# Kernel tuning notes

Measured on AMD Instinct MI355X. Metric: run time of the kernel, lower is better.

Reference implementation:

```python
import jax, jax.numpy as jnp
import numpy as np

NA, NT = 50000, 100000          # address / transaction node counts
FA, FT = 128, 64                # raw feature dims per node type
HID, OUT, HEADS, NCLS = 128, 64, 8, 2
E1, E2 = 500000, 250000         # cross-type / same-type edge counts
NEG_SLOPE = 0.2
LN_EPS = 1e-5


def _edge_att(xs, xd, src, dst, a_s, a_d, n_dst):
    # xs: [Ns,H,D] projected src feats, xd: [Nd,H,D] projected dst feats
    alpha_s = (xs * a_s).sum(-1)                     # [Ns,H]
    alpha_d = (xd * a_d).sum(-1)                     # [Nd,H]
    alpha = alpha_s[src] + alpha_d[dst]              # [E,H]
    alpha = jnp.where(alpha > 0, alpha, NEG_SLOPE * alpha)  # leaky_relu(0.2)
    # segment softmax over incoming edges of each dst node
    m = jax.lax.stop_gradient(jax.ops.segment_max(alpha, dst, num_segments=n_dst))
    m = jnp.where(jnp.isfinite(m), m, 0.0)
    ex = jnp.exp(alpha - m[dst])
    denom = jax.ops.segment_sum(ex, dst, num_segments=n_dst)
    w = ex / jnp.maximum(denom[dst], 1e-16)          # [E,H]
    msg = xs[src] * w[:, :, None]                    # [E,H,D]
    out = jax.ops.segment_sum(msg, dst, num_segments=n_dst)
    return jax.nn.relu(out.reshape(n_dst, -1))       # [Nd, H*D] (HANConv relu per edge type)


def _group(outs, q, kW, kb):
    # semantic-level attention over metapaths; outs: [K,N,F]
    score = (jnp.tanh(outs @ kW + kb).mean(axis=1) * q).sum(-1)  # [K]
    attn = jax.nn.softmax(score)
    return jnp.einsum('k,knf->nf', attn, outs)


def _layer_norm(x, g, b):
    mu = x.mean(-1, keepdims=True)
    var = ((x - mu) ** 2).mean(-1, keepdims=True)
    return (x - mu) / jnp.sqrt(var + LN_EPS) * g + b


def _han_conv(xa, xt, edges, Wa, ba, Wt, bt, atts, q, kW, kb):
    C = Wa.shape[1]
    D = C // HEADS
    za = (xa @ Wa + ba).reshape(-1, HEADS, D)
    zt = (xt @ Wt + bt).reshape(-1, HEADS, D)
    (eat_s, eat_d), (eta_s, eta_d), (eaa_s, eaa_d), (ett_s, ett_d) = edges
    (as_at, ad_at), (as_ta, ad_ta), (as_aa, ad_aa), (as_tt, ad_tt) = atts
    o_at = _edge_att(za, zt, eat_s, eat_d, as_at, ad_at, zt.shape[0])  # -> transaction
    o_ta = _edge_att(zt, za, eta_s, eta_d, as_ta, ad_ta, za.shape[0])  # -> address
    o_aa = _edge_att(za, za, eaa_s, eaa_d, as_aa, ad_aa, za.shape[0])  # -> address
    o_tt = _edge_att(zt, zt, ett_s, ett_d, as_tt, ad_tt, zt.shape[0])  # -> transaction
    new_a = _group(jnp.stack([o_ta, o_aa]), q, kW, kb)
    new_t = _group(jnp.stack([o_at, o_tt]), q, kW, kb)
    return new_a, new_t


def _forward(x_address, x_transaction,
             W_a1, b_a1, W_t1, b_t1,
             as_at1, ad_at1, as_ta1, ad_ta1, as_aa1, ad_aa1, as_tt1, ad_tt1,
             k1_W, k1_b, q1,
             W_a2, b_a2, W_t2, b_t2,
             as_at2, ad_at2, as_ta2, ad_ta2, as_aa2, ad_aa2, as_tt2, ad_tt2,
             k2_W, k2_b, q2,
             ln1_g, ln1_b, ln2_g, ln2_b, lin_W, lin_b, edges):
    atts1 = ((as_at1, ad_at1), (as_ta1, ad_ta1), (as_aa1, ad_aa1), (as_tt1, ad_tt1))
    atts2 = ((as_at2, ad_at2), (as_ta2, ad_ta2), (as_aa2, ad_aa2), (as_tt2, ad_tt2))
    xa, xt = _han_conv(x_address, x_transaction, edges, W_a1, b_a1, W_t1, b_t1, atts1, q1, k1_W, k1_b)
    xa = jax.nn.relu(_layer_norm(xa, ln1_g, ln1_b))
    xt = jax.nn.relu(_layer_norm(xt, ln1_g, ln1_b))
    # dropout is identity in eval mode
    xa, xt = _han_conv(xa, xt, edges, W_a2, b_a2, W_t2, b_t2, atts2, q2, k2_W, k2_b)
    xa = jax.nn.relu(_layer_norm(xa, ln2_g, ln2_b))
    return xa @ lin_W + lin_b                          # [NA, NCLS]


def setup_inputs() -> dict:
    key = jax.random.key(0)
    ks = jax.random.split(key, 40)
    D1, D2 = HID // HEADS, OUT // HEADS
    def n(i, shape, s=0.1):
        return jax.random.normal(ks[i], shape, jnp.float32) * s
    inp = {
        'x_address': jax.random.normal(ks[0], (NA, FA), jnp.float32),
        'x_transaction': jax.random.normal(ks[1], (NT, FT), jnp.float32),
        'eat_src': jax.random.randint(ks[2], (E1,), 0, NA),
        'eat_dst': jax.random.randint(ks[3], (E1,), 0, NT),
        'eta_src': jax.random.randint(ks[4], (E1,), 0, NT),
        'eta_dst': jax.random.randint(ks[5], (E1,), 0, NA),
        'eaa_src': jax.random.randint(ks[6], (E2,), 0, NA),
        'eaa_dst': jax.random.randint(ks[7], (E2,), 0, NA),
        'ett_src': jax.random.randint(ks[8], (E2,), 0, NT),
        'ett_dst': jax.random.randint(ks[9], (E2,), 0, NT),
        'W_a1': n(10, (FA, HID)), 'b_a1': jnp.zeros((HID,), jnp.float32),
        'W_t1': n(11, (FT, HID)), 'b_t1': jnp.zeros((HID,), jnp.float32),
        'as_at1': n(12, (HEADS, D1)), 'ad_at1': n(13, (HEADS, D1)),
        'as_ta1': n(14, (HEADS, D1)), 'ad_ta1': n(15, (HEADS, D1)),
        'as_aa1': n(16, (HEADS, D1)), 'ad_aa1': n(17, (HEADS, D1)),
        'as_tt1': n(18, (HEADS, D1)), 'ad_tt1': n(19, (HEADS, D1)),
        'k1_W': n(20, (HID, HID)), 'k1_b': jnp.zeros((HID,), jnp.float32), 'q1': n(21, (HID,)),
        'W_a2': n(22, (HID, OUT)), 'b_a2': jnp.zeros((OUT,), jnp.float32),
        'W_t2': n(23, (HID, OUT)), 'b_t2': jnp.zeros((OUT,), jnp.float32),
        'as_at2': n(24, (HEADS, D2)), 'ad_at2': n(25, (HEADS, D2)),
        'as_ta2': n(26, (HEADS, D2)), 'ad_ta2': n(27, (HEADS, D2)),
        'as_aa2': n(28, (HEADS, D2)), 'ad_aa2': n(29, (HEADS, D2)),
        'as_tt2': n(30, (HEADS, D2)), 'ad_tt2': n(31, (HEADS, D2)),
        'k2_W': n(32, (OUT, OUT)), 'k2_b': jnp.zeros((OUT,), jnp.float32), 'q2': n(33, (OUT,)),
        'ln1_g': jnp.ones((HID,), jnp.float32), 'ln1_b': jnp.zeros((HID,), jnp.float32),
        'ln2_g': jnp.ones((OUT,), jnp.float32), 'ln2_b': jnp.zeros((OUT,), jnp.float32),
        'lin_W': n(34, (OUT, NCLS)), 'lin_b': jnp.zeros((NCLS,), jnp.float32),
    }
    return inp


def reference(x_address, x_transaction,
              eat_src, eat_dst, eta_src, eta_dst, eaa_src, eaa_dst, ett_src, ett_dst,
              W_a1, b_a1, W_t1, b_t1,
              as_at1, ad_at1, as_ta1, ad_ta1, as_aa1, ad_aa1, as_tt1, ad_tt1,
              k1_W, k1_b, q1,
              W_a2, b_a2, W_t2, b_t2,
              as_at2, ad_at2, as_ta2, ad_ta2, as_aa2, ad_aa2, as_tt2, ad_tt2,
              k2_W, k2_b, q2,
              ln1_g, ln1_b, ln2_g, ln2_b, lin_W, lin_b):
    edges = ((eat_src, eat_dst), (eta_src, eta_dst), (eaa_src, eaa_dst), (ett_src, ett_dst))
    return _forward(x_address, x_transaction,
                    W_a1, b_a1, W_t1, b_t1,
                    as_at1, ad_at1, as_ta1, ad_ta1, as_aa1, ad_aa1, as_tt1, ad_tt1,
                    k1_W, k1_b, q1,
                    W_a2, b_a2, W_t2, b_t2,
                    as_at2, ad_at2, as_ta2, ad_ta2, as_aa2, ad_aa2, as_tt2, ad_tt2,
                    k2_W, k2_b, q2,
                    ln1_g, ln1_b, ln2_g, ln2_b, lin_W, lin_b, edges)
```

## Files before the change

kernel.cpp:

```cpp
#include <hip/hip_runtime.h>
#include <cstdint>
#include <cstddef>
#include <type_traits>

#define NA 50000
#define NT 100000
#define FA 128
#define FT 64
#define HID 128
#define OUTF 64
#define HEADS 8
#define E1 500000
#define E2 250000
#define NTOT (2*NT + 2*NA)
#define ETOT (2*E1 + 2*E2)
#define NSH 8

typedef __attribute__((ext_vector_type(8))) short short8;
typedef __attribute__((ext_vector_type(4))) float f32x4;

static __device__ __forceinline__ ushort f2b(float f) {
  unsigned int u = __float_as_uint(f);
  return (ushort)((u + 0x7fffu + ((u >> 16) & 1u)) >> 16);
}
static __device__ __forceinline__ float b2f(ushort b) {
  return __uint_as_float(((unsigned int)b) << 16);
}
static __device__ __forceinline__ float u2f_lo(unsigned int u) {
  return __uint_as_float(u << 16);
}
static __device__ __forceinline__ float u2f_hi(unsigned int u) {
  return __uint_as_float(u & 0xffff0000u);
}

template<int KK>
static __device__ __forceinline__ int lidx(int row, int off) {
  return row * KK + (off ^ ((row & 7) << 3));
}

template<int KK, int M>
static __device__ __forceinline__ void stageB(const float* __restrict__ W,
                                              ushort* __restrict__ Bls)
{
  constexpr int TPC = 256 / M;
  constexpr int CH  = KK / TPC;
  constexpr int BL  = (CH < 16) ? CH : 16;
  int t = threadIdx.x;
  int col = t % M;
  int k0 = (t / M) * CH;
  const float* Wp = W + col;
#pragma unroll
  for (int b = 0; b < CH; b += BL) {
    float v[BL];
#pragma unroll
    for (int i = 0; i < BL; i++) v[i] = Wp[(size_t)(k0 + b + i) * M];
#pragma unroll
    for (int q = 0; q < BL / 8; q++) {
      union { ushort u[8]; uint4 x; } p;
#pragma unroll
      for (int i = 0; i < 8; i++) p.u[i] = f2b(v[q * 8 + i]);
      *reinterpret_cast<uint4*>(&Bls[lidx<KK>(col, k0 + b + q * 8)]) = p.x;
    }
  }
}

template<int KK, typename AT>
struct ARegs {
  float4 f[std::is_same<AT, float>::value ? KK / 16 : 1];
  uint4  u[std::is_same<AT, float>::value ? 1 : KK / 32];
};

template<int KK, typename AT>
static __device__ __forceinline__ void loadA(const AT* __restrict__ A, int N,
                                             int row0, ARegs<KK, AT>& R)
{
  int t = threadIdx.x;
  int arow = t >> 2, ac0 = (t & 3) * (KK / 4);
  int row = row0 + arow;
  bool ok = row < N;
  const AT* Ap = A + (size_t)row * KK + ac0;
  if constexpr (std::is_same<AT, float>::value) {
#pragma unroll
    for (int j = 0; j < KK / 16; j++)
      R.f[j] = ok ? *reinterpret_cast<const float4*>(Ap + j * 4)
                  : make_float4(0.f, 0.f, 0.f, 0.f);
  } else {
#pragma unroll
    for (int j = 0; j < KK / 32; j++)
      R.u[j] = ok ? *reinterpret_cast<const uint4*>(Ap + j * 8)
                  : make_uint4(0, 0, 0, 0);
  }
}

template<int KK, typename AT>
static __device__ __forceinline__ void writeA(const ARegs<KK, AT>& R,
                                              ushort* __restrict__ Als)
{
  int t = threadIdx.x;
  int arow = t >> 2, ac0 = (t & 3) * (KK / 4);
#pragma unroll
  for (int j = 0; j < KK / 32; j++) {
    uint4 w;
    if constexpr (std::is_same<AT, float>::value) {
      union { ushort u[8]; uint4 x; } p;
      float4 a0 = R.f[2 * j], a1 = R.f[2 * j + 1];
      p.u[0] = f2b(a0.x); p.u[1] = f2b(a0.y); p.u[2] = f2b(a0.z); p.u[3] = f2b(a0.w);
      p.u[4] = f2b(a1.x); p.u[5] = f2b(a1.y); p.u[6] = f2b(a1.z); p.u[7] = f2b(a1.w);
      w = p.x;
    } else {
      w = R.u[j];
    }
    *reinterpret_cast<uint4*>(&Als[lidx<KK>(arow, ac0 + j * 8)]) = w;
  }
}

template<int KK, int NCT>
static __device__ __forceinline__ void mfma_tile(const ushort* __restrict__ Als,
    const ushort* __restrict__ Bls, f32x4* acc)
{
  int lane = threadIdx.x & 63, w = threadIdx.x >> 6;
  int l15 = lane & 15, l4 = lane >> 4;
#pragma unroll
  for (int ks = 0; ks < KK / 32; ks++) {
    short8 af = *reinterpret_cast<const short8*>(
        &Als[lidx<KK>(16 * w + l15, ks * 32 + l4 * 8)]);
#pragma unroll
    for (int n = 0; n < NCT; n++) {
      short8 bf = *reinterpret_cast<const short8*>(
          &Bls[lidx<KK>(16 * n + l15, ks * 32 + l4 * 8)]);
      acc[n] = __builtin_amdgcn_mfma_f32_16x16x32_bf16(af, bf, acc[n], 0, 0, 0);
    }
  }
}

template<int NV, int DD, int KK, int M, int TPB, typename AT>
__global__ __launch_bounds__(256) void zgemm_k(
    const AT* __restrict__ A, const float* __restrict__ W,
    const float* __restrict__ bias,
    const float* __restrict__ v0, const float* __restrict__ v1,
    const float* __restrict__ v2, const float* __restrict__ v3,
    float* __restrict__ o0, float* __restrict__ o1,
    float* __restrict__ o2, float* __restrict__ o3,
    ushort* __restrict__ Cb, int N)
{
  constexpr int NCT = M / 16;
  __shared__ __align__(16) ushort Bls[M * KK];
  __shared__ __align__(16) ushort Als[64 * KK];
  int t = threadIdx.x, w = t >> 6, lane = t & 63;
  int l15 = lane & 15, l4 = lane >> 4;
  int ntiles = (N + 63) >> 6;
  int tile0 = blockIdx.x * TPB;
  int nt = min(TPB, ntiles - tile0);

  stageB<KK, M>(W, Bls);
  ARegs<KK, AT> R;
  loadA<KK, AT>(A, N, tile0 * 64, R);

  float bv[NCT], aw0[NCT], aw1[NCT], aw2[NCT], aw3[NCT];
#pragma unroll
  for (int n = 0; n < NCT; n++) {
    int col = 16 * n + l15;
    bv[n] = bias[col];
    int head = (DD == 16) ? n : (n * 2 + (l15 >> 3));
    int vi = head * DD + (l15 & (DD - 1));
    aw0[n] = v0[vi];
    aw1[n] = (NV > 1) ? v1[vi] : 0.f;
    aw2[n] = (NV > 2) ? v2[vi] : 0.f;
    aw3[n] = (NV > 3) ? v3[vi] : 0.f;
  }

  for (int i = 0; i < nt; i++) {
    int row0 = (tile0 + i) * 64;
    __syncthreads();
    writeA<KK, AT>(R, Als);
    __syncthreads();
    if (i + 1 < nt) loadA<KK, AT>(A, N, row0 + 64, R);
    f32x4 acc[NCT];
#pragma unroll
    for (int n = 0; n < NCT; n++) acc[n] = (f32x4){0.f, 0.f, 0.f, 0.f};
    mfma_tile<KK, NCT>(Als, Bls, acc);

#pragma unroll
    for (int n = 0; n < NCT; n++) {
      int col = 16 * n + l15;
      int head = (DD == 16) ? n : (n * 2 + (l15 >> 3));
#pragma unroll
      for (int r = 0; r < 4; r++) {
        int row = row0 + 16 * w + l4 * 4 + r;
        float v = acc[n][r] + bv[n];
        if (row < N) Cb[(size_t)row * M + col] = f2b(v);
        float a0 = v * aw0[n], a1 = v * aw1[n], a2 = v * aw2[n], a3 = v * aw3[n];
#pragma unroll
        for (int o = 1; o < DD; o <<= 1) {
          a0 += __shfl_xor(a0, o);
          if (NV > 1) a1 += __shfl_xor(a1, o);
          if (NV > 2) a2 += __shfl_xor(a2, o);
          if (NV > 3) a3 += __shfl_xor(a3, o);
        }
        if ((l15 & (DD - 1)) == 0 && row < N) {
          o0[(size_t)row * 8 + head] = a0;
          if (NV > 1) o1[(size_t)row * 8 + head] = a1;
          if (NV > 2) o2[(size_t)row * 8 + head] = a2;
          if (NV > 3) o3[(size_t)row * 8 + head] = a3;
        }
      }
    }
  }
}

template<int KK, int M, int TPB>
__global__ __launch_bounds__(256) void score_k(
    const ushort* __restrict__ A0, const ushort* __restrict__ A1,
    const ushort* __restrict__ A2, const ushort* __restrict__ A3,
    const float* __restrict__ W, const float* __restrict__ bias,
    const float* __restrict__ qv, float* __restrict__ scp,
    int4 cumB, int4 Ns)
{
  constexpr int NCT = M / 16;
  __shared__ __align__(16) ushort Bls[M * KK];
  __shared__ __align__(16) ushort Als[64 * KK];
  __shared__ float red[4];
  int b = blockIdx.x;
  int tsk, bbase, N; const ushort* A;
  if      (b < cumB.x) { tsk = 0; bbase = 0;      N = Ns.x; A = A0; }
  else if (b < cumB.y) { tsk = 1; bbase = cumB.x; N = Ns.y; A = A1; }
  else if (b < cumB.z) { tsk = 2; bbase = cumB.y; N = Ns.z; A = A2; }
  else                 { tsk = 3; bbase = cumB.z; N = Ns.w; A = A3; }
  int t = threadIdx.x, w = t >> 6, lane = t & 63;
  int l15 = lane & 15, l4 = lane >> 4;
  int ntiles = (N + 63) >> 6;
  int tile0 = (b - bbase) * TPB;
  int nt = min(TPB, ntiles - tile0);

  stageB<KK, M>(W, Bls);
  ARegs<KK, ushort> R;
  loadA<KK, ushort>(A, N, tile0 * 64, R);

  float bb[NCT], qb[NCT];
#pragma unroll
  for (int n = 0; n < NCT; n++) {
    int col = 16 * n + l15;
    bb[n] = bias[col]; qb[n] = qv[col];
  }

  float ls = 0.f;
  for (int i = 0; i < nt; i++) {
    int row0 = (tile0 + i) * 64;
    __syncthreads();
    writeA<KK, ushort>(R, Als);
    __syncthreads();
    if (i + 1 < nt) loadA<KK, ushort>(A, N, row0 + 64, R);
    f32x4 acc[NCT];
#pragma unroll
    for (int n = 0; n < NCT; n++) acc[n] = (f32x4){0.f, 0.f, 0.f, 0.f};
    mfma_tile<KK, NCT>(Als, Bls, acc);
#pragma unroll
    for (int n = 0; n < NCT; n++) {
#pragma unroll
      for (int r = 0; r < 4; r++) {
        int row = row0 + 16 * w + l4 * 4 + r;
        if (row < N) ls += tanhf(acc[n][r] + bb[n]) * qb[n];
      }
    }
  }
#pragma unroll
  for (int o = 32; o > 0; o >>= 1) ls += __shfl_xor(ls, o);
  if (lane == 0) red[w] = ls;
  __syncthreads();
  if (t == 0) atomicAdd(&scp[tsk], red[0] + red[1] + red[2] + red[3]);
}

__global__ void hist4_sh(const int* __restrict__ d0, const int* __restrict__ d1,
    const int* __restrict__ d2, const int* __restrict__ d3,
    int* __restrict__ cnt8, float* __restrict__ scp)
{
  if (blockIdx.x == 0 && threadIdx.x < 8) scp[threadIdx.x] = 0.f;
  int e = blockIdx.x * 256 + threadIdx.x;
  int sh = blockIdx.x & (NSH - 1);
  int d;
  if      (e < E1)          d = d0[e];
  else if (e < 2*E1)        d = d1[e - E1] + NT;
  else if (e < 2*E1 + E2)   d = d2[e - 2*E1] + NT + NA;
  else if (e < ETOT)        d = d3[e - 2*E1 - E2] + NT + 2*NA;
  else return;
  atomicAdd(&cnt8[sh * NTOT + d], 1);
}

__global__ void scatter_sh(const int* __restrict__ s0, const int* __restrict__ d0,
    const int* __restrict__ s1, const int* __restrict__ d1,
    const int* __restrict__ s2, const int* __restrict__ d2,
    const int* __restrict__ s3, const int* __restrict__ d3,
    int* __restrict__ cur8, int* __restrict__ ssh)
{
  int e = blockIdx.x * 256 + threadIdx.x;
  int sh = blockIdx.x & (NSH - 1);
  int d, s;
  if      (e < E1)          { d = d0[e];                           s = s0[e]; }
  else if (e < 2*E1)        { d = d1[e - E1] + NT;                 s = s1[e - E1]; }
  else if (e < 2*E1 + E2)   { d = d2[e - 2*E1] + NT + NA;          s = s2[e - 2*E1]; }
  else if (e < ETOT)        { d = d3[e - 2*E1 - E2] + NT + 2*NA;   s = s3[e - 2*E1 - E2]; }
  else return;
  int p = atomicAdd(&cur8[sh * NTOT + d], 1);
  ssh[p] = s;
}

__global__ void sumsh_k(const int* __restrict__ cnt8, int* __restrict__ cnt)
{
  int g = blockIdx.x * 256 + threadIdx.x;
  if (g >= NTOT) return;
  int s = 0;
#pragma unroll
  for (int k = 0; k < NSH; k++) s += cnt8[k * NTOT + g];
  cnt[g] = s;
}

__global__ void compact_k(const int* __restrict__ rp8, const int* __restrict__ rp,
    const int* __restrict__ ssh, int* __restrict__ ssrc)
{
  int g = blockIdx.x * 256 + threadIdx.x;
  if (g >= NTOT) return;
  int w = rp[g];
#pragma unroll
  for (int s = 0; s < NSH; s++) {
    int b0 = rp8[s * NTOT + g], b1 = rp8[s * NTOT + g + 1];
    for (int e = b0; e < b1; e++) ssrc[w++] = ssh[e];
  }
}

__global__ __launch_bounds__(256) void scan_blk(const int* __restrict__ in,
    int* __restrict__ rp1, int* __restrict__ bsum, int n)
{
  __shared__ int sh[256];
  int base = blockIdx.x * 2048;
  int t = threadIdx.x;
  int v[8]; int s = 0;
#pragma unroll
  for (int k = 0; k < 8; k++) {
    int i = base + t * 8 + k;
    v[k] = (i < n) ? in[i] : 0; s += v[k];
  }
  sh[t] = s; __syncthreads();
  for (int o = 1; o < 256; o <<= 1) {
    int x = (t >= o) ? sh[t - o] : 0;
    __syncthreads(); sh[t] += x; __syncthreads();
  }
  int run = (t == 0) ? 0 : sh[t - 1];
  if (t == 255 && bsum) bsum[blockIdx.x] = sh[255];
#pragma unroll
  for (int k = 0; k < 8; k++) {
    int i = base + t * 8 + k;
    run += v[k];
    if (i < n) rp1[i] = run;
  }
}

__global__ void scan_add2(int* __restrict__ rp, int* __restrict__ cur,
    const int* __restrict__ bsA, int n)
{
  int i = blockIdx.x * blockDim.x + threadIdx.x;
  if (i == 0) { rp[0] = 0; cur[0] = 0; }
  if (i < n) {
    int blk = i >> 11;
    int base = blk ? bsA[blk - 1] : 0;
    int v = rp[i + 1] + base;
    rp[i + 1] = v;
    if (i + 1 < n) cur[i + 1] = v;
  }
}

__global__ void scan_add(int* __restrict__ rp, const int* __restrict__ bsA, int n)
{
  int i = blockIdx.x * blockDim.x + threadIdx.x;
  if (i == 0) rp[0] = 0;
  if (i < n) {
    int blk = i >> 11;
    int base = blk ? bsA[blk - 1] : 0;
    rp[i + 1] += base;
  }
}

struct AggTask {
  int g0, Nd;
  const float* als; const float* ald;
  const ushort* z;  ushort* out;
};

template<int F>
__global__ __launch_bounds__(256) void agg_multi(const int* __restrict__ rp,
    const int* __restrict__ ssrc, AggTask T0, AggTask T1, AggTask T2, AggTask T3,
    int c1, int c2, int c3)
{
  constexpr int LPN = (F == 128) ? 16 : 8;
  constexpr int NPW = 64 / LPN;
  int b = blockIdx.x;
  AggTask T; int lb;
  if      (b < c1) { T = T0; lb = b; }
  else if (b < c2) { T = T1; lb = b - c1; }
  else if (b < c3) { T = T2; lb = b - c2; }
  else             { T = T3; lb = b - c3; }
  int wv = threadIdx.x >> 6, lane = threadIdx.x & 63;
  int grp = lane / LPN, lg = lane % LPN;
  int n = (lb * 4 + wv) * NPW + grp;
  if (n >= T.Nd) return;
  int g = T.g0 + n;
  int start = rp[g], end = rp[g + 1];
  int hh = (F == 128) ? (lg >> 1) : lg;
  float ad_h = T.ald[(size_t)n * 8 + hh];

  float den = 0.f;
  float acc[8] = {};
  for (int e = start; e < end; e++) {
    int sn = ssrc[e];
    uint4 zv = *reinterpret_cast<const uint4*>(T.z + (size_t)sn * F + lg * 8);
    float a = T.als[(size_t)sn * 8 + hh] + ad_h;
    a = a > 0.f ? a : 0.2f * a;
    float p = __expf(fminf(a, 30.f));
    den += p;
    acc[0] = fmaf(p, u2f_lo(zv.x), acc[0]);
    acc[1] = fmaf(p, u2f_hi(zv.x), acc[1]);
    acc[2] = fmaf(p, u2f_lo(zv.y), acc[2]);
    acc[3] = fmaf(p, u2f_hi(zv.y), acc[3]);
    acc[4] = fmaf(p, u2f_lo(zv.z), acc[4]);
    acc[5] = fmaf(p, u2f_hi(zv.z), acc[5]);
    acc[6] = fmaf(p, u2f_lo(zv.w), acc[6]);
    acc[7] = fmaf(p, u2f_hi(zv.w), acc[7]);
  }
  float inv = 1.f / fmaxf(den, 1e-16f);
  unsigned int pk[4];
#pragma unroll
  for (int k2 = 0; k2 < 4; k2++)
    pk[k2] = (unsigned int)f2b(fmaxf(acc[2*k2] * inv, 0.f))
           | ((unsigned int)f2b(fmaxf(acc[2*k2+1] * inv, 0.f)) << 16);
  *reinterpret_cast<uint4*>(T.out + (size_t)n * F + lg * 8)
      = make_uint4(pk[0], pk[1], pk[2], pk[3]);
}

__global__ __launch_bounds__(256) void combine2_k(
    const ushort* __restrict__ o00, const ushort* __restrict__ o01,
    const float* __restrict__ sc0, float invn0, ushort* __restrict__ out0, int N0,
    const ushort* __restrict__ o10, const ushort* __restrict__ o11,
    const float* __restrict__ sc1, float invn1, ushort* __restrict__ out1, int N1,
    const float* __restrict__ g, const float* __restrict__ bb)
{
  int c1 = (N0 + 3) / 4;
  int b = blockIdx.x;
  const ushort *o0, *o1; const float* sc; float invn; ushort* outp; int N, lb;
  if (b < c1) { o0=o00; o1=o01; sc=sc0; invn=invn0; outp=out0; N=N0; lb=b; }
  else        { o0=o10; o1=o11; sc=sc1; invn=invn1; outp=out1; N=N1; lb=b-c1; }
  int wv = threadIdx.x >> 6, lane = threadIdx.x & 63;
  int n = lb * 4 + wv;
  if (n >= N) return;
  float s0 = sc[0] * invn, s1 = sc[1] * invn;
  float mx = fmaxf(s0, s1);
  float e0 = __expf(s0 - mx), e1 = __expf(s1 - mx);
  float w0 = e0 / (e0 + e1), w1 = e1 / (e0 + e1);
  float x[2];
#pragma unroll
  for (int jj = 0; jj < 2; jj++) {
    int idx = lane + 64 * jj;
    x[jj] = w0 * b2f(o0[(size_t)n * 128 + idx]) + w1 * b2f(o1[(size_t)n * 128 + idx]);
  }
  float sum = x[0] + x[1];
#pragma unroll
  for (int o = 32; o > 0; o >>= 1) sum += __shfl_xor(sum, o);
  float mu = sum / 128.f;
  float vs = 0.f;
#pragma unroll
  for (int jj = 0; jj < 2; jj++) { float dd = x[jj] - mu; vs = fmaf(dd, dd, vs); }
#pragma unroll
  for (int o = 32; o > 0; o >>= 1) vs += __shfl_xor(vs, o);
  float rstd = rsqrtf(vs / 128.f + 1e-5f);
#pragma unroll
  for (int jj = 0; jj < 2; jj++) {
    int idx = lane + 64 * jj;
    float y = (x[jj] - mu) * rstd * g[idx] + bb[idx];
    outp[(size_t)n * 128 + idx] = f2b(fmaxf(y, 0.f));
  }
}

__global__ __launch_bounds__(256) void combine_final_k(
    const ushort* __restrict__ o0, const ushort* __restrict__ o1,
    const float* __restrict__ sc, float invn,
    const float* __restrict__ g, const float* __restrict__ bb,
    const float* __restrict__ lw, const float* __restrict__ lb,
    float* __restrict__ outp, int N)
{
  int wv = threadIdx.x >> 6, lane = threadIdx.x & 63;
  int n = blockIdx.x * 4 + wv;
  if (n >= N) return;
  float s0 = sc[0] * invn, s1 = sc[1] * invn;
  float mx = fmaxf(s0, s1);
  float e0 = __expf(s0 - mx), e1 = __expf(s1 - mx);
  float w0 = e0 / (e0 + e1), w1 = e1 / (e0 + e1);
  float x = w0 * b2f(o0[(size_t)n * 64 + lane]) + w1 * b2f(o1[(size_t)n * 64 + lane]);
  float sum = x;
#pragma unroll
  for (int o = 32; o > 0; o >>= 1) sum += __shfl_xor(sum, o);
  float mu = sum / 64.f;
  float dd = x - mu;
  float vs = dd * dd;
#pragma unroll
  for (int o = 32; o > 0; o >>= 1) vs += __shfl_xor(vs, o);
  float rstd = rsqrtf(vs / 64.f + 1e-5f);
  float y = fmaxf((x - mu) * rstd * g[lane] + bb[lane], 0.f);
  float p0 = y * lw[lane * 2 + 0];
  float p1 = y * lw[lane * 2 + 1];
#pragma unroll
  for (int o = 32; o > 0; o >>= 1) { p0 += __shfl_xor(p0, o); p1 += __shfl_xor(p1, o); }
  if (lane == 0) {
    outp[(size_t)n * 2 + 0] = p0 + lb[0];
    outp[(size_t)n * 2 + 1] = p1 + lb[1];
  }
}

extern "C" void kernel_launch(void* const* d_in, const int* in_sizes, int n_in,
                              void* d_out, int out_size, void* d_ws, size_t ws_size,
                              hipStream_t stream)
{
  (void)in_sizes; (void)n_in; (void)out_size;
  const float* x_a = (const float*)d_in[0];
  const float* x_t = (const float*)d_in[1];
  const int* eat_s = (const int*)d_in[2];
  const int* eat_d = (const int*)d_in[3];
  const int* eta_s = (const int*)d_in[4];
  const int* eta_d = (const int*)d_in[5];
  const int* eaa_s = (const int*)d_in[6];
  const int* eaa_d = (const int*)d_in[7];
  const int* ett_s = (const int*)d_in[8];
  const int* ett_d = (const int*)d_in[9];
  const float* W_a1 = (const float*)d_in[10]; const float* b_a1 = (const float*)d_in[11];
  const float* W_t1 = (const float*)d_in[12]; const float* b_t1 = (const float*)d_in[13];
  const float* as_at1 = (const float*)d_in[14]; const float* ad_at1 = (const float*)d_in[15];
  const float* as_ta1 = (const float*)d_in[16]; const float* ad_ta1 = (const float*)d_in[17];
  const float* as_aa1 = (const float*)d_in[18]; const float* ad_aa1 = (const float*)d_in[19];
  const float* as_tt1 = (const float*)d_in[20]; const float* ad_tt1 = (const float*)d_in[21];
  const float* k1_W = (const float*)d_in[22]; const float* k1_b = (const float*)d_in[23];
  const float* q1   = (const float*)d_in[24];
  const float* W_a2 = (const float*)d_in[25]; const float* b_a2 = (const float*)d_in[26];
  const float* W_t2 = (const float*)d_in[27]; const float* b_t2 = (const float*)d_in[28];
  const float* as_ta2 = (const float*)d_in[31]; const float* ad_ta2 = (const float*)d_in[32];
  const float* as_aa2 = (const float*)d_in[33]; const float* ad_aa2 = (const float*)d_in[34];
  const float* k2_W = (const float*)d_in[37]; const float* k2_b = (const float*)d_in[38];
  const float* q2   = (const float*)d_in[39];
  const float* ln1_g = (const float*)d_in[40]; const float* ln1_b = (const float*)d_in[41];
  const float* ln2_g = (const float*)d_in[42]; const float* ln2_b = (const float*)d_in[43];
  const float* lin_W = (const float*)d_in[44]; const float* lin_b = (const float*)d_in[45];

  char* ws = (char*)d_ws;
  size_t off = 0;
  auto alloc = [&](size_t bytes) {
    size_t o = off; off += (bytes + 255) & ~(size_t)255; return o;
  };
  size_t ZA1 = alloc((size_t)NA * HID * 2);
  size_t ZT1 = alloc((size_t)NT * HID * 2);
  size_t OTA = alloc((size_t)NA * HID * 2);
  size_t OAA = alloc((size_t)NA * HID * 2);
  size_t OAT = alloc((size_t)NT * HID * 2);
  size_t OTT = alloc((size_t)NT * HID * 2);
  size_t A_AS_AT = alloc((size_t)NA * 8 * 4);
  size_t A_AD_TA = alloc((size_t)NA * 8 * 4);
  size_t A_AS_AA = alloc((size_t)NA * 8 * 4);
  size_t A_AD_AA = alloc((size_t)NA * 8 * 4);
  size_t A_T_D_AT = alloc((size_t)NT * 8 * 4);
  size_t A_T_S_TA = alloc((size_t)NT * 8 * 4);
  size_t A_T_S_TT = alloc((size_t)NT * 8 * 4);
  size_t A_T_D_TT = alloc((size_t)NT * 8 * 4);
  size_t RP8  = alloc(((size_t)NSH * NTOT + 1) * 4);
  size_t CUR8 = alloc((size_t)NSH * NTOT * 4);
  size_t SSH  = alloc((size_t)ETOT * 4);
  size_t RP   = alloc((size_t)(NTOT + 1) * 4);
  size_t CNT  = alloc((size_t)NTOT * 4);
  size_t SS   = alloc((size_t)ETOT * 4);
  size_t BSM  = alloc(2048 * 4);
  size_t BSM2 = alloc(256 * 4);
  size_t SC   = alloc(256);
  if (off > ws_size) return;

  ushort* za1 = (ushort*)(ws + ZA1);
  ushort* zt1 = (ushort*)(ws + ZT1);
  ushort* ota = (ushort*)(ws + OTA);
  ushort* oaa = (ushort*)(ws + OAA);
  ushort* oat = (ushort*)(ws + OAT);
  ushort* ott = (ushort*)(ws + OTT);
  float* aASAT = (float*)(ws + A_AS_AT);
  float* aADTA = (float*)(ws + A_AD_TA);
  float* aASAA = (float*)(ws + A_AS_AA);
  float* aADAA = (float*)(ws + A_AD_AA);
  float* aTDAT = (float*)(ws + A_T_D_AT);
  float* aTSTA = (float*)(ws + A_T_S_TA);
  float* aTSTT = (float*)(ws + A_T_S_TT);
  float* aTDTT = (float*)(ws + A_T_D_TT);
  int* rp8  = (int*)(ws + RP8);
  int* cur8 = (int*)(ws + CUR8);
  int* ssh  = (int*)(ws + SSH);
  int* rp   = (int*)(ws + RP);
  int* cnt  = (int*)(ws + CNT);
  int* ssrc = (int*)(ws + SS);
  int* bsum = (int*)(ws + BSM);
  int* bsum2= (int*)(ws + BSM2);
  float* scp = (float*)(ws + SC);
  ushort* za2 = za1;
  ushort* zt2 = zt1;
  ushort* ota2 = oaa;
  ushort* oaa2 = (ushort*)(ws + OAA + (size_t)NA * OUTF * 2);

  const int TA = (NA + 63) / 64, TT = (NT + 63) / 64;
  const int EBL = (ETOT + 255) / 256;
  const int SCN8 = NSH * NTOT;
  const int SBL8 = (SCN8 + 2047) / 2048;
  const int SBL1 = (NTOT + 2047) / 2048;

  hipMemsetAsync(cur8, 0, (size_t)SCN8 * 4, stream);
  hist4_sh<<<EBL, 256, 0, stream>>>(eat_d, eta_d, eaa_d, ett_d, cur8, scp);
  sumsh_k<<<(NTOT + 255) / 256, 256, 0, stream>>>(cur8, cnt);
  scan_blk<<<SBL8, 256, 0, stream>>>(cur8, rp8 + 1, bsum, SCN8);
  scan_blk<<<1, 256, 0, stream>>>(bsum, bsum, nullptr, SBL8);
  scan_add2<<<(SCN8 + 255) / 256, 256, 0, stream>>>(rp8, cur8, bsum, SCN8);
  scan_blk<<<SBL1, 256, 0, stream>>>(cnt, rp + 1, bsum2, NTOT);
  scan_blk<<<1, 256, 0, stream>>>(bsum2, bsum2, nullptr, SBL1);
  scan_add<<<(NTOT + 255) / 256, 256, 0, stream>>>(rp, bsum2, NTOT);
  scatter_sh<<<EBL, 256, 0, stream>>>(eat_s, eat_d, eta_s, eta_d,
                                      eaa_s, eaa_d, ett_s, ett_d, cur8, ssh);
  compact_k<<<(NTOT + 255) / 256, 256, 0, stream>>>(rp8, rp, ssh, ssrc);

  zgemm_k<4,16,FA,HID,2,float><<<(TA+1)/2,256,0,stream>>>(x_a, W_a1, b_a1,
      as_at1, ad_ta1, as_aa1, ad_aa1, aASAT, aADTA, aASAA, aADAA, za1, NA);
  zgemm_k<4,16,FT,HID,4,float><<<(TT+3)/4,256,0,stream>>>(x_t, W_t1, b_t1,
      ad_at1, as_ta1, as_tt1, ad_tt1, aTDAT, aTSTA, aTSTT, aTDTT, zt1, NT);
  {
    const int BT = (NT + 15) / 16, BA = (NA + 15) / 16;
    AggTask T0{0,          NT, aASAT, aTDAT, za1, oat};
    AggTask T1{NT,         NA, aTSTA, aADTA, zt1, ota};
    AggTask T2{NT+NA,      NA, aASAA, aADAA, za1, oaa};
    AggTask T3{NT+2*NA,    NT, aTSTT, aTDTT, zt1, ott};
    agg_multi<128><<<2*BT + 2*BA, 256, 0, stream>>>(rp, ssrc,
        T0, T1, T2, T3, BT, BT + BA, BT + 2*BA);
  }
  {
    const int bA = (TA + 3) / 4, bT = (TT + 3) / 4;
    score_k<HID,HID,4><<<2*bA + 2*bT, 256, 0, stream>>>(ota, oaa, oat, ott,
        k1_W, k1_b, q1, scp,
        make_int4(bA, 2*bA, 2*bA + bT, 2*bA + 2*bT),
        make_int4(NA, NA, NT, NT));
  }
  combine2_k<<<(NA/4) + (NT/4), 256, 0, stream>>>(
      ota, oaa, scp + 0, 1.f/NA, ota, NA,
      oat, ott, scp + 2, 1.f/NT, oat, NT, ln1_g, ln1_b);

  zgemm_k<3,8,HID,OUTF,2,ushort><<<(TA+1)/2,256,0,stream>>>(ota, W_a2, b_a2,
      ad_ta2, as_aa2, ad_aa2, nullptr, aADTA, aASAA, aADAA, nullptr, za2, NA);
  zgemm_k<1,8,HID,OUTF,4,ushort><<<(TT+3)/4,256,0,stream>>>(oat, W_t2, b_t2,
      as_ta2, nullptr, nullptr, nullptr, aTSTA, nullptr, nullptr, nullptr, zt2, NT);
  {
    const int BA2 = (NA + 31) / 32;
    AggTask T0{NT,    NA, aTSTA, aADTA, zt2, ota2};
    AggTask T1{NT+NA, NA, aASAA, aADAA, za2, oaa2};
    agg_multi<64><<<2*BA2, 256, 0, stream>>>(rp, ssrc,
        T0, T1, T1, T1, BA2, 2*BA2, 2*BA2);
  }
  {
    const int bA = (TA + 3) / 4;
    score_k<OUTF,OUTF,4><<<2*bA, 256, 0, stream>>>(ota2, oaa2, ota2, ota2,
        k2_W, k2_b, q2, scp + 4,
        make_int4(bA, 2*bA, 2*bA, 2*bA),
        make_int4(NA, NA, NA, NA));
  }
  combine_final_k<<<NA/4, 256, 0, stream>>>(ota2, oaa2, scp + 4, 1.f/NA,
      ln2_g, ln2_b, lin_W, lin_b, (float*)d_out, NA);
}
```

Baseline: 518.4 us.

## Fuse shard-sum into scan, merge block-sum scans, interleave aggregation tasks, unroll edges

The separate shard-count summation kernel is folded into the block scan, and the two single-block scans of block sums are merged into one two-block launch, removing launches and a temporary count buffer. The aggregation kernel now interleaves blocks reading za and zt in groups of four, so concurrently running blocks gather from both source tensors. This aims to balance cache and memory traffic across the source tables. The edge loop is also unrolled by two so two gathers are in flight per iteration, at the cost of more registers.

New measurement: 519.0 us. About the same (+0.1%).

```diff
diff --git a/kernel.cpp b/kernel.cpp
--- a/kernel.cpp
+++ b/kernel.cpp
@@ -304,16 +304,6 @@
   ssh[p] = s;
 }
 
-__global__ void sumsh_k(const int* __restrict__ cnt8, int* __restrict__ cnt)
-{
-  int g = blockIdx.x * 256 + threadIdx.x;
-  if (g >= NTOT) return;
-  int s = 0;
-#pragma unroll
-  for (int k = 0; k < NSH; k++) s += cnt8[k * NTOT + g];
-  cnt[g] = s;
-}
-
 __global__ void compact_k(const int* __restrict__ rp8, const int* __restrict__ rp,
     const int* __restrict__ ssh, int* __restrict__ ssrc)
 {
@@ -351,6 +341,65 @@
     int i = base + t * 8 + k;
     run += v[k];
     if (i < n) rp1[i] = run;
+  }
+}
+
+__global__ __launch_bounds__(256) void scan_blk_sum8(const int* __restrict__ cnt8,
+    int* __restrict__ rp1, int* __restrict__ bsum, int n)
+{
+  __shared__ int sh[256];
+  int base = blockIdx.x * 2048;
+  int t = threadIdx.x;
+  int v[8]; int s = 0;
+#pragma unroll
+  for (int k = 0; k < 8; k++) {
+    int i = base + t * 8 + k;
+    int x = 0;
+    if (i < n) {
+#pragma unroll
+      for (int sh2 = 0; sh2 < NSH; sh2++) x += cnt8[sh2 * NTOT + i];
+    }
+    v[k] = x; s += x;
+  }
+  sh[t] = s; __syncthreads();
+  for (int o = 1; o < 256; o <<= 1) {
+    int x = (t >= o) ? sh[t - o] : 0;
+    __syncthreads(); sh[t] += x; __syncthreads();
+  }
+  int run = (t == 0) ? 0 : sh[t - 1];
+  if (t == 255 && bsum) bsum[blockIdx.x] = sh[255];
+#pragma unroll
+  for (int k = 0; k < 8; k++) {
+    int i = base + t * 8 + k;
+    run += v[k];
+    if (i < n) rp1[i] = run;
+  }
+}
+
+__global__ __launch_bounds__(256) void scan_two(int* __restrict__ b0, int n0,
+                                                int* __restrict__ b1, int n1)
+{
+  __shared__ int sh[256];
+  int* arr = blockIdx.x ? b1 : b0;
+  int n = blockIdx.x ? n1 : n0;
+  int t = threadIdx.x;
+  int v[8]; int s = 0;
+#pragma unroll
+  for (int k = 0; k < 8; k++) {
+    int i = t * 8 + k;
+    v[k] = (i < n) ? arr[i] : 0; s += v[k];
+  }
+  sh[t] = s; __syncthreads();
+  for (int o = 1; o < 256; o <<= 1) {
+    int x = (t >= o) ? sh[t - o] : 0;
+    __syncthreads(); sh[t] += x; __syncthreads();
+  }
+  int run = (t == 0) ? 0 : sh[t - 1];
+#pragma unroll
+  for (int k = 0; k < 8; k++) {
+    int i = t * 8 + k;
+    run += v[k];
+    if (i < n) arr[i] = run;
   }
 }
 
@@ -387,17 +436,18 @@
 
 template<int F>
 __global__ __launch_bounds__(256) void agg_multi(const int* __restrict__ rp,
-    const int* __restrict__ ssrc, AggTask T0, AggTask T1, AggTask T2, AggTask T3,
-    int c1, int c2, int c3)
+    const int* __restrict__ ssrc, AggTask C0A, AggTask C0B,
+    AggTask C1A, AggTask C1B, int split0, int split1, int btot)
 {
   constexpr int LPN = (F == 128) ? 16 : 8;
   constexpr int NPW = 64 / LPN;
   int b = blockIdx.x;
-  AggTask T; int lb;
-  if      (b < c1) { T = T0; lb = b; }
-  else if (b < c2) { T = T1; lb = b - c1; }
-  else if (b < c3) { T = T2; lb = b - c2; }
-  else             { T = T3; lb = b - c3; }
+  int cls = (b >> 2) & 1;
+  int lb = (b >> 3) * 4 + (b & 3);
+  if (lb >= btot) return;
+  AggTask T;
+  if (cls == 0) { if (lb < split0) T = C0A; else { T = C0B; lb -= split0; } }
+  else          { if (lb < split1) T = C1A; else { T = C1B; lb -= split1; } }
   int wv = threadIdx.x >> 6, lane = threadIdx.x & 63;
   int grp = lane / LPN, lg = lane % LPN;
   int n = (lb * 4 + wv) * NPW + grp;
@@ -409,7 +459,28 @@
 
   float den = 0.f;
   float acc[8] = {};
-  for (int e = start; e < end; e++) {
+  int e = start;
+  for (; e + 1 < end; e += 2) {
+    int sn0 = ssrc[e], sn1 = ssrc[e + 1];
+    uint4 z0 = *reinterpret_cast<const uint4*>(T.z + (size_t)sn0 * F + lg * 8);
+    uint4 z1 = *reinterpret_cast<const uint4*>(T.z + (size_t)sn1 * F + lg * 8);
+    float a0 = T.als[(size_t)sn0 * 8 + hh] + ad_h;
+    float a1 = T.als[(size_t)sn1 * 8 + hh] + ad_h;
+    a0 = a0 > 0.f ? a0 : 0.2f * a0;
+    a1 = a1 > 0.f ? a1 : 0.2f * a1;
+    float p0 = __expf(fminf(a0, 30.f));
+    float p1 = __expf(fminf(a1, 30.f));
+    den += p0 + p1;
+    acc[0] = fmaf(p0, u2f_lo(z0.x), fmaf(p1, u2f_lo(z1.x), acc[0]));
+    acc[1] = fmaf(p0, u2f_hi(z0.x), fmaf(p1, u2f_hi(z1.x), acc[1]));
+    acc[2] = fmaf(p0, u2f_lo(z0.y), fmaf(p1, u2f_lo(z1.y), acc[2]));
+    acc[3] = fmaf(p0, u2f_hi(z0.y), fmaf(p1, u2f_hi(z1.y), acc[3]));
+    acc[4] = fmaf(p0, u2f_lo(z0.z), fmaf(p1, u2f_lo(z1.z), acc[4]));
+    acc[5] = fmaf(p0, u2f_hi(z0.z), fmaf(p1, u2f_hi(z1.z), acc[5]));
+    acc[6] = fmaf(p0, u2f_lo(z0.w), fmaf(p1, u2f_lo(z1.w), acc[6]));
+    acc[7] = fmaf(p0, u2f_hi(z0.w), fmaf(p1, u2f_hi(z1.w), acc[7]));
+  }
+  if (e < end) {
     int sn = ssrc[e];
     uint4 zv = *reinterpret_cast<const uint4*>(T.z + (size_t)sn * F + lg * 8);
     float a = T.als[(size_t)sn * 8 + hh] + ad_h;
@@ -569,7 +640,6 @@
   size_t CUR8 = alloc((size_t)NSH * NTOT * 4);
   size_t SSH  = alloc((size_t)ETOT * 4);
   size_t RP   = alloc((size_t)(NTOT + 1) * 4);
-  size_t CNT  = alloc((size_t)NTOT * 4);
   size_t SS   = alloc((size_t)ETOT * 4);
   size_t BSM  = alloc(2048 * 4);
   size_t BSM2 = alloc(256 * 4);
@@ -594,7 +664,6 @@
   int* cur8 = (int*)(ws + CUR8);
   int* ssh  = (int*)(ws + SSH);
   int* rp   = (int*)(ws + RP);
-  int* cnt  = (int*)(ws + CNT);
   int* ssrc = (int*)(ws + SS);
   int* bsum = (int*)(ws + BSM);
   int* bsum2= (int*)(ws + BSM2);
@@ -612,12 +681,10 @@
 
   hipMemsetAsync(cur8, 0, (size_t)SCN8 * 4, stream);
   hist4_sh<<<EBL, 256, 0, stream>>>(eat_d, eta_d, eaa_d, ett_d, cur8, scp);
-  sumsh_k<<<(NTOT + 255) / 256, 256, 0, stream>>>(cur8, cnt);
   scan_blk<<<SBL8, 256, 0, stream>>>(cur8, rp8 + 1, bsum, SCN8);
-  scan_blk<<<1, 256, 0, stream>>>(bsum, bsum, nullptr, SBL8);
+  scan_blk_sum8<<<SBL1, 256, 0, stream>>>(cur8, rp + 1, bsum2, NTOT);
+  scan_two<<<2, 256, 0, stream>>>(bsum, SBL8, bsum2, SBL1);
   scan_add2<<<(SCN8 + 255) / 256, 256, 0, stream>>>(rp8, cur8, bsum, SCN8);
-  scan_blk<<<SBL1, 256, 0, stream>>>(cnt, rp + 1, bsum2, NTOT);
-  scan_blk<<<1, 256, 0, stream>>>(bsum2, bsum2, nullptr, SBL1);
   scan_add<<<(NTOT + 255) / 256, 256, 0, stream>>>(rp, bsum2, NTOT);
   scatter_sh<<<EBL, 256, 0, stream>>>(eat_s, eat_d, eta_s, eta_d,
                                       eaa_s, eaa_d, ett_s, ett_d, cur8, ssh);
@@ -629,12 +696,14 @@
       ad_at1, as_ta1, as_tt1, ad_tt1, aTDAT, aTSTA, aTSTT, aTDTT, zt1, NT);
   {
     const int BT = (NT + 15) / 16, BA = (NA + 15) / 16;
-    AggTask T0{0,          NT, aASAT, aTDAT, za1, oat};
-    AggTask T1{NT,         NA, aTSTA, aADTA, zt1, ota};
-    AggTask T2{NT+NA,      NA, aASAA, aADAA, za1, oaa};
-    AggTask T3{NT+2*NA,    NT, aTSTT, aTDTT, zt1, ott};
-    agg_multi<128><<<2*BT + 2*BA, 256, 0, stream>>>(rp, ssrc,
-        T0, T1, T2, T3, BT, BT + BA, BT + 2*BA);
+    const int btot = BT + BA;
+    const int grid = ((btot + 3) / 4) * 8;
+    AggTask Tat{0,        NT, aASAT, aTDAT, za1, oat};
+    AggTask Taa{NT+NA,    NA, aASAA, aADAA, za1, oaa};
+    AggTask Tta{NT,       NA, aTSTA, aADTA, zt1, ota};
+    AggTask Ttt{NT+2*NA,  NT, aTSTT, aTDTT, zt1, ott};
+    agg_multi<128><<<grid, 256, 0, stream>>>(rp, ssrc,
+        Tat, Taa, Tta, Ttt, BT, BA, btot);
   }
   {
     const int bA = (TA + 3) / 4, bT = (TT + 3) / 4;
@@ -653,10 +722,11 @@
       as_ta2, nullptr, nullptr, nullptr, aTSTA, nullptr, nullptr, nullptr, zt2, NT);
   {
     const int BA2 = (NA + 31) / 32;
-    AggTask T0{NT,    NA, aTSTA, aADTA, zt2, ota2};
-    AggTask T1{NT+NA, NA, aASAA, aADAA, za2, oaa2};
-    agg_multi<64><<<2*BA2, 256, 0, stream>>>(rp, ssrc,
-        T0, T1, T1, T1, BA2, 2*BA2, 2*BA2);
+    const int grid = ((BA2 + 3) / 4) * 8;
+    AggTask Taa2{NT+NA, NA, aASAA, aADAA, za2, oaa2};
+    AggTask Tta2{NT,    NA, aTSTA, aADTA, zt2, ota2};
+    agg_multi<64><<<grid, 256, 0, stream>>>(rp, ssrc,
+        Taa2, Taa2, Tta2, Tta2, BA2, BA2, BA2);
   }
   {
     const int bA = (TA + 3) / 4;
```
